# Performance work log

Measured on AMD Instinct MI355X. Metric: run time of the kernel, lower is better.

The kernel has to match this reference:

```python
import jax, jax.numpy as jnp
import numpy as np

WIDTH = [512, 512, 512, 512]
GRID_SIZE = 5
K = 3  # spline order
GRID_RANGE = (-1.0, 1.0)
BATCH = 1024


def extend_grid(grid, k):
    # grid: (I, G+1) -> (I, G+2k+1), extend k knots on each side with uniform step h
    h = (grid[:, -1:] - grid[:, :1]) / (grid.shape[1] - 1)
    for _ in range(k):
        grid = jnp.concatenate([grid[:, :1] - h, grid, grid[:, -1:] + h], axis=1)
    return grid


def b_spline_basis(x, grid, k):
    # Cox-de Boor recursion. x: (B, I), grid: (I, G+2k+1) -> (B, I, G+k)
    xe = x[:, :, None]
    g = grid[None, :, :]
    B = ((xe >= g[:, :, :-1]) & (xe < g[:, :, 1:])).astype(x.dtype)
    for p in range(1, k + 1):
        B = ((xe - g[:, :, :-(p + 1)]) / (g[:, :, p:-1] - g[:, :, :-(p + 1)]) * B[:, :, :-1]
             + (g[:, :, p + 1:] - xe) / (g[:, :, p + 1:] - g[:, :, 1:-p]) * B[:, :, 1:])
    return B


def kan_layer(x, grid, coef, sb, sp):
    # x: (B, I); coef: (I, O, G+k); sb, sp: (I, O)
    base = jax.nn.silu(x)                              # residual b(x), (B, I)
    Bmat = b_spline_basis(x, grid, K)                  # (B, I, G+k)
    y = jnp.einsum('bik,iok->bio', Bmat, coef)         # spline curves, (B, I, O)
    post = sb[None] * base[:, :, None] + sp[None] * y  # postacts (B, I, O)
    return post.sum(axis=1)                            # (B, O)


def setup_inputs() -> dict:
    key = jax.random.key(0)
    ks = jax.random.split(key, 1 + 2 * (len(WIDTH) - 1))
    inp = {"x": jax.random.normal(ks[0], (BATCH, WIDTH[0]), dtype=jnp.float32)}
    for l, (i, o) in enumerate(zip(WIDTH[:-1], WIDTH[1:])):
        base = jnp.linspace(GRID_RANGE[0], GRID_RANGE[1], GRID_SIZE + 1, dtype=jnp.float32)
        grid = extend_grid(jnp.broadcast_to(base[None], (i, GRID_SIZE + 1)), K)
        kc, kb = ks[1 + 2 * l], ks[2 + 2 * l]
        inp[f"grid{l}"] = grid
        inp[f"coef{l}"] = jax.random.normal(kc, (i, o, GRID_SIZE + K), dtype=jnp.float32) * (0.1 / GRID_SIZE)
        inp[f"sb{l}"] = (jax.random.uniform(kb, (i, o), dtype=jnp.float32) * 2.0 - 1.0) / np.sqrt(i).astype(np.float32)
        inp[f"sp{l}"] = jnp.ones((i, o), dtype=jnp.float32) / np.sqrt(i).astype(np.float32)
    return inp


def reference(x, grid0, coef0, sb0, sp0, grid1, coef1, sb1, sp1, grid2, coef2, sb2, sp2):
    x = kan_layer(x, grid0, coef0, sb0, sp0)
    x = kan_layer(x, grid1, coef1, sb1, sp1)
    x = kan_layer(x, grid2, coef2, sb2, sp2)
    return x
```

## Files before the change

kernel.cpp:

```cpp
#include <hip/hip_runtime.h>
#include <hip/hip_bf16.h>

#define I_DIM  512
#define O_DIM  512
#define NBATCH 1024
#define NSPL   8
#define KPI    12
#define KDIM   (I_DIM * KPI)
#define NGRID  12

typedef __attribute__((ext_vector_type(8))) short bf16x8;
typedef __attribute__((ext_vector_type(4))) float f32x4;

__device__ __forceinline__ void gload_lds16(const __hip_bfloat16* g, __hip_bfloat16* l) {
    __builtin_amdgcn_global_load_lds(
        (const __attribute__((address_space(1))) void*)g,
        (__attribute__((address_space(3))) void*)l, 16, 0, 0);
}

__global__ void build_wt_all(const float* __restrict__ c0, const float* __restrict__ b0, const float* __restrict__ p0,
                             const float* __restrict__ c1, const float* __restrict__ b1, const float* __restrict__ p1,
                             const float* __restrict__ c2, const float* __restrict__ b2, const float* __restrict__ p2,
                             __hip_bfloat16* __restrict__ Wt) {
    int l = blockIdx.y;
    const float* coef = l == 0 ? c0 : (l == 1 ? c1 : c2);
    const float* sb   = l == 0 ? b0 : (l == 1 ? b1 : b2);
    const float* sp   = l == 0 ? p0 : (l == 1 ? p1 : p2);
    __hip_bfloat16* W = Wt + (size_t)l * O_DIM * KDIM;

    int tid = blockIdx.x * blockDim.x + threadIdx.x;
    int i = tid & (I_DIM - 1);
    int o = tid >> 9;
    float sbv = sb[i * O_DIM + o];
    float spv = sp[i * O_DIM + o];
    const float* cf = coef + (size_t)(i * O_DIM + o) * NSPL;
    __align__(16) __hip_bfloat16 row[KPI];
#pragma unroll
    for (int k = 0; k < NSPL; ++k) row[k] = __float2bfloat16(spv * cf[k]);
    __hip_bfloat16 whi = __float2bfloat16(sbv);
    __hip_bfloat16 wlo = __float2bfloat16(sbv - __bfloat162float(whi));
    row[8]  = whi;
    row[9]  = wlo;
    row[10] = whi;
    row[11] = __float2bfloat16(0.0f);
    uint2* dst = (uint2*)(W + (size_t)o * KDIM + i * KPI);
    const uint2* src = (const uint2*)row;
    dst[0] = src[0]; dst[1] = src[1]; dst[2] = src[2];
}

#define SPLITK 8

__device__ __forceinline__ void features_core(float xv, const float* __restrict__ grid,
                                              int i, __hip_bfloat16* __restrict__ dst) {
    float g[NGRID];
#pragma unroll
    for (int j = 0; j < NGRID; ++j) g[j] = grid[i * NGRID + j];

    float B[NGRID - 1];
#pragma unroll
    for (int j = 0; j < NGRID - 1; ++j)
        B[j] = (xv >= g[j] && xv < g[j + 1]) ? 1.0f : 0.0f;
#pragma unroll
    for (int p = 1; p <= 3; ++p) {
#pragma unroll
        for (int j = 0; j < NGRID - 1 - p; ++j) {
            B[j] = (xv - g[j]) / (g[j + p] - g[j]) * B[j]
                 + (g[j + p + 1] - xv) / (g[j + p + 1] - g[j + 1]) * B[j + 1];
        }
    }
    float s = xv / (1.0f + __expf(-xv));
    __hip_bfloat16 shi = __float2bfloat16(s);
    __hip_bfloat16 slo = __float2bfloat16(s - __bfloat162float(shi));

    __align__(16) __hip_bfloat16 row[KPI];
#pragma unroll
    for (int k = 0; k < NSPL; ++k) row[k] = __float2bfloat16(B[k]);
    row[8]  = shi;
    row[9]  = shi;
    row[10] = slo;
    row[11] = __float2bfloat16(0.0f);

    uint2* d = (uint2*)dst;
    const uint2* srow = (const uint2*)row;
    d[0] = srow[0]; d[1] = srow[1]; d[2] = srow[2];
}

__global__ void build_features_x(const float* __restrict__ x,
                                 const float* __restrict__ grid,
                                 __hip_bfloat16* __restrict__ F) {
    int tid = blockIdx.x * blockDim.x + threadIdx.x;
    features_core(x[tid], grid, tid & (I_DIM - 1), F + (size_t)tid * KPI);
}

__global__ void build_features_sum(const float* __restrict__ P,
                                   const float* __restrict__ grid,
                                   __hip_bfloat16* __restrict__ F) {
    int tid = blockIdx.x * blockDim.x + threadIdx.x;
    float xv = 0.f;
#pragma unroll
    for (int s = 0; s < SPLITK; ++s) xv += P[(size_t)s * NBATCH * I_DIM + tid];
    features_core(xv, grid, tid & (I_DIM - 1), F + (size_t)tid * KPI);
}

__global__ void reduce_out(const float* __restrict__ P, float* __restrict__ out) {
    int tid = blockIdx.x * blockDim.x + threadIdx.x;
    float v = 0.f;
#pragma unroll
    for (int s = 0; s < SPLITK; ++s) v += P[(size_t)s * NBATCH * O_DIM + tid];
    out[tid] = v;
}

#define BM 64
#define BN 64
#define BK 64
#define KSEG (KDIM / SPLITK)

__global__ __launch_bounds__(256)
void gemm_kernel(const __hip_bfloat16* __restrict__ A,
                 const __hip_bfloat16* __restrict__ Wt,
                 float* __restrict__ P) {
    __shared__ __hip_bfloat16 lA[BM * BK];
    __shared__ __hip_bfloat16 lB[BN * BK];

    int bm = blockIdx.x;
    int bn = blockIdx.y;
    int ks = blockIdx.z;
    int tid = threadIdx.x;
    int lane = tid & 63;
    int wave = tid >> 6;
    int wr = (wave & 1) * 32;
    int wc = (wave >> 1) * 32;
    int q  = lane >> 4;
    int ln = lane & 15;

    f32x4 acc[2][2];
#pragma unroll
    for (int a = 0; a < 2; ++a)
#pragma unroll
        for (int b = 0; b < 2; ++b) acc[a][b] = (f32x4){0.f, 0.f, 0.f, 0.f};

    const __hip_bfloat16* Abase = A  + (size_t)(bm * BM) * KDIM + ks * KSEG;
    const __hip_bfloat16* Bbase = Wt + (size_t)(bn * BN) * KDIM + ks * KSEG;

    int cc0 = wave * 128 + lane;
    int cc1 = cc0 + 64;
    int r0 = cc0 >> 3, j0 = (cc0 & 7) ^ (r0 & 7);
    int r1 = cc1 >> 3, j1 = (cc1 & 7) ^ (r1 & 7);
    __hip_bfloat16* ldsA0 = lA + (size_t)(wave * 128) * 8;
    __hip_bfloat16* ldsA1 = lA + (size_t)(wave * 128 + 64) * 8;
    __hip_bfloat16* ldsB0 = lB + (size_t)(wave * 128) * 8;
    __hip_bfloat16* ldsB1 = lB + (size_t)(wave * 128 + 64) * 8;

    for (int kt = 0; kt < KSEG; kt += BK) {
        __syncthreads();
        gload_lds16(Abase + (size_t)r0 * KDIM + kt + j0 * 8, ldsA0);
        gload_lds16(Abase + (size_t)r1 * KDIM + kt + j1 * 8, ldsA1);
        gload_lds16(Bbase + (size_t)r0 * KDIM + kt + j0 * 8, ldsB0);
        gload_lds16(Bbase + (size_t)r1 * KDIM + kt + j1 * 8, ldsB1);
        __syncthreads();

#pragma unroll
        for (int kh = 0; kh < 2; ++kh) {
            bf16x8 af[2], bfr[2];
#pragma unroll
            for (int rt = 0; rt < 2; ++rt) {
                int row = wr + rt * 16 + ln;
                af[rt] = *(const bf16x8*)(lA + row * BK + (((kh * 4 + q) ^ (row & 7)) * 8));
            }
#pragma unroll
            for (int ct = 0; ct < 2; ++ct) {
                int row = wc + ct * 16 + ln;
                bfr[ct] = *(const bf16x8*)(lB + row * BK + (((kh * 4 + q) ^ (row & 7)) * 8));
            }
#pragma unroll
            for (int rt = 0; rt < 2; ++rt)
#pragma unroll
                for (int ct = 0; ct < 2; ++ct)
                    acc[rt][ct] = __builtin_amdgcn_mfma_f32_16x16x32_bf16(
                        af[rt], bfr[ct], acc[rt][ct], 0, 0, 0);
        }
    }

    float* Pp = P + (size_t)ks * NBATCH * O_DIM;
    int orow = bm * BM + wr;
    int ocol = bn * BN + wc + ln;
#pragma unroll
    for (int rt = 0; rt < 2; ++rt)
#pragma unroll
        for (int ct = 0; ct < 2; ++ct)
#pragma unroll
            for (int r = 0; r < 4; ++r)
                Pp[(size_t)(orow + rt * 16 + q * 4 + r) * O_DIM + ocol + ct * 16]
                    = acc[rt][ct][r];
}

extern "C" void kernel_launch(void* const* d_in, const int* in_sizes, int n_in,
                              void* d_out, int out_size, void* d_ws, size_t ws_size,
                              hipStream_t stream) {
    const float* x0      = (const float*)d_in[0];
    const float* grid[3] = {(const float*)d_in[1], (const float*)d_in[5], (const float*)d_in[9]};
    const float* coef[3] = {(const float*)d_in[2], (const float*)d_in[6], (const float*)d_in[10]};
    const float* sb[3]   = {(const float*)d_in[3], (const float*)d_in[7], (const float*)d_in[11]};
    const float* sp[3]   = {(const float*)d_in[4], (const float*)d_in[8], (const float*)d_in[12]};

    char* ws = (char*)d_ws;
    const size_t wt_bytes = (size_t)O_DIM * KDIM * sizeof(__hip_bfloat16);
    const size_t f_bytes  = (size_t)NBATCH * KDIM * sizeof(__hip_bfloat16);
    __hip_bfloat16* Wt = (__hip_bfloat16*)ws;
    __hip_bfloat16* F  = (__hip_bfloat16*)(ws + 3 * wt_bytes);
    float* P = (float*)(ws + 3 * wt_bytes + f_bytes);

    build_wt_all<<<dim3((I_DIM * O_DIM) / 256, 3), 256, 0, stream>>>(
        coef[0], sb[0], sp[0], coef[1], sb[1], sp[1], coef[2], sb[2], sp[2], Wt);

    build_features_x<<<(NBATCH * I_DIM) / 256, 256, 0, stream>>>(x0, grid[0], F);
    gemm_kernel<<<dim3(16, 8, SPLITK), 256, 0, stream>>>(F, Wt, P);

    for (int l = 1; l < 3; ++l) {
        build_features_sum<<<(NBATCH * I_DIM) / 256, 256, 0, stream>>>(P, grid[l], F);
        gemm_kernel<<<dim3(16, 8, SPLITK), 256, 0, stream>>>(F, Wt + (size_t)l * O_DIM * KDIM, P);
    }
    reduce_out<<<(NBATCH * O_DIM) / 256, 256, 0, stream>>>(P, (float*)d_out);
}
```

Before: 201.3 us.

## Enlarge GEMM tiles to 128x128, double split-K, fuse prep kernels

The GEMM block tile grows from 64x64 to 128x128, with each wave computing a 4x4 grid of MFMA tiles instead of 2x2, so each loaded fragment is reused more. Split-K is raised from 8 to 16 to keep enough blocks (8x4x16) in flight. The weight-build and first-layer feature kernels are merged into one launch. In exchange the partial-sum buffer P doubles, so the reduction passes read twice as much. The larger tile also raises register use and may lower occupancy.

```diff
diff --git a/kernel.cpp b/kernel.cpp
--- a/kernel.cpp
+++ b/kernel.cpp
@@ -8,6 +8,7 @@
 #define KPI    12
 #define KDIM   (I_DIM * KPI)
 #define NGRID  12
+#define SPLITK 16
 
 typedef __attribute__((ext_vector_type(8))) short bf16x8;
 typedef __attribute__((ext_vector_type(4))) float f32x4;
@@ -18,17 +19,10 @@
         (__attribute__((address_space(3))) void*)l, 16, 0, 0);
 }
 
-__global__ void build_wt_all(const float* __restrict__ c0, const float* __restrict__ b0, const float* __restrict__ p0,
-                             const float* __restrict__ c1, const float* __restrict__ b1, const float* __restrict__ p1,
-                             const float* __restrict__ c2, const float* __restrict__ b2, const float* __restrict__ p2,
-                             __hip_bfloat16* __restrict__ Wt) {
-    int l = blockIdx.y;
-    const float* coef = l == 0 ? c0 : (l == 1 ? c1 : c2);
-    const float* sb   = l == 0 ? b0 : (l == 1 ? b1 : b2);
-    const float* sp   = l == 0 ? p0 : (l == 1 ? p1 : p2);
-    __hip_bfloat16* W = Wt + (size_t)l * O_DIM * KDIM;
-
-    int tid = blockIdx.x * blockDim.x + threadIdx.x;
+__device__ __forceinline__ void wt_core(const float* __restrict__ coef,
+                                        const float* __restrict__ sb,
+                                        const float* __restrict__ sp,
+                                        __hip_bfloat16* __restrict__ W, int tid) {
     int i = tid & (I_DIM - 1);
     int o = tid >> 9;
     float sbv = sb[i * O_DIM + o];
@@ -48,8 +42,6 @@
     dst[0] = src[0]; dst[1] = src[1]; dst[2] = src[2];
 }
 
-#define SPLITK 8
-
 __device__ __forceinline__ void features_core(float xv, const float* __restrict__ grid,
                                               int i, __hip_bfloat16* __restrict__ dst) {
     float g[NGRID];
@@ -85,11 +77,23 @@
     d[0] = srow[0]; d[1] = srow[1]; d[2] = srow[2];
 }
 
-__global__ void build_features_x(const float* __restrict__ x,
-                                 const float* __restrict__ grid,
-                                 __hip_bfloat16* __restrict__ F) {
-    int tid = blockIdx.x * blockDim.x + threadIdx.x;
-    features_core(x[tid], grid, tid & (I_DIM - 1), F + (size_t)tid * KPI);
+__global__ void prep_kernel(const float* __restrict__ c0, const float* __restrict__ b0, const float* __restrict__ p0,
+                            const float* __restrict__ c1, const float* __restrict__ b1, const float* __restrict__ p1,
+                            const float* __restrict__ c2, const float* __restrict__ b2, const float* __restrict__ p2,
+                            __hip_bfloat16* __restrict__ Wt,
+                            const float* __restrict__ x, const float* __restrict__ grid0,
+                            __hip_bfloat16* __restrict__ F) {
+    if (blockIdx.x < 3072) {
+        int l = blockIdx.x / 1024;
+        const float* coef = l == 0 ? c0 : (l == 1 ? c1 : c2);
+        const float* sb   = l == 0 ? b0 : (l == 1 ? b1 : b2);
+        const float* sp   = l == 0 ? p0 : (l == 1 ? p1 : p2);
+        int tid = (blockIdx.x - l * 1024) * 256 + threadIdx.x;
+        wt_core(coef, sb, sp, Wt + (size_t)l * O_DIM * KDIM, tid);
+    } else {
+        int tid = (blockIdx.x - 3072) * 256 + threadIdx.x;
+        features_core(x[tid], grid0, tid & (I_DIM - 1), F + (size_t)tid * KPI);
+    }
 }
 
 __global__ void build_features_sum(const float* __restrict__ P,
@@ -110,8 +114,8 @@
     out[tid] = v;
 }
 
-#define BM 64
-#define BN 64
+#define BM 128
+#define BN 128
 #define BK 64
 #define KSEG (KDIM / SPLITK)
 
@@ -128,56 +132,58 @@
     int tid = threadIdx.x;
     int lane = tid & 63;
     int wave = tid >> 6;
-    int wr = (wave & 1) * 32;
-    int wc = (wave >> 1) * 32;
+    int wr = (wave & 1) * 64;
+    int wc = (wave >> 1) * 64;
     int q  = lane >> 4;
     int ln = lane & 15;
 
-    f32x4 acc[2][2];
-#pragma unroll
-    for (int a = 0; a < 2; ++a)
-#pragma unroll
-        for (int b = 0; b < 2; ++b) acc[a][b] = (f32x4){0.f, 0.f, 0.f, 0.f};
+    f32x4 acc[4][4];
+#pragma unroll
+    for (int a = 0; a < 4; ++a)
+#pragma unroll
+        for (int b = 0; b < 4; ++b) acc[a][b] = (f32x4){0.f, 0.f, 0.f, 0.f};
 
     const __hip_bfloat16* Abase = A  + (size_t)(bm * BM) * KDIM + ks * KSEG;
     const __hip_bfloat16* Bbase = Wt + (size_t)(bn * BN) * KDIM + ks * KSEG;
 
-    int cc0 = wave * 128 + lane;
-    int cc1 = cc0 + 64;
-    int r0 = cc0 >> 3, j0 = (cc0 & 7) ^ (r0 & 7);
-    int r1 = cc1 >> 3, j1 = (cc1 & 7) ^ (r1 & 7);
-    __hip_bfloat16* ldsA0 = lA + (size_t)(wave * 128) * 8;
-    __hip_bfloat16* ldsA1 = lA + (size_t)(wave * 128 + 64) * 8;
-    __hip_bfloat16* ldsB0 = lB + (size_t)(wave * 128) * 8;
-    __hip_bfloat16* ldsB1 = lB + (size_t)(wave * 128 + 64) * 8;
+    int ccw[4], rr[4], jj[4];
+#pragma unroll
+    for (int c = 0; c < 4; ++c) {
+        int cc = c * 256 + tid;
+        ccw[c] = c * 256 + wave * 64;
+        rr[c] = cc >> 3;
+        jj[c] = (cc & 7) ^ (rr[c] & 7);
+    }
 
     for (int kt = 0; kt < KSEG; kt += BK) {
         __syncthreads();
-        gload_lds16(Abase + (size_t)r0 * KDIM + kt + j0 * 8, ldsA0);
-        gload_lds16(Abase + (size_t)r1 * KDIM + kt + j1 * 8, ldsA1);
-        gload_lds16(Bbase + (size_t)r0 * KDIM + kt + j0 * 8, ldsB0);
-        gload_lds16(Bbase + (size_t)r1 * KDIM + kt + j1 * 8, ldsB1);
+#pragma unroll
+        for (int c = 0; c < 4; ++c)
+            gload_lds16(Abase + (size_t)rr[c] * KDIM + kt + jj[c] * 8, lA + ccw[c] * 8);
+#pragma unroll
+        for (int c = 0; c < 4; ++c)
+            gload_lds16(Bbase + (size_t)rr[c] * KDIM + kt + jj[c] * 8, lB + ccw[c] * 8);
         __syncthreads();
 
 #pragma unroll
         for (int kh = 0; kh < 2; ++kh) {
-            bf16x8 af[2], bfr[2];
-#pragma unroll
-            for (int rt = 0; rt < 2; ++rt) {
+            bf16x8 af[4], bf[4];
+#pragma unroll
+            for (int rt = 0; rt < 4; ++rt) {
                 int row = wr + rt * 16 + ln;
                 af[rt] = *(const bf16x8*)(lA + row * BK + (((kh * 4 + q) ^ (row & 7)) * 8));
             }
 #pragma unroll
-            for (int ct = 0; ct < 2; ++ct) {
+            for (int ct = 0; ct < 4; ++ct) {
                 int row = wc + ct * 16 + ln;
-                bfr[ct] = *(const bf16x8*)(lB + row * BK + (((kh * 4 + q) ^ (row & 7)) * 8));
+                bf[ct] = *(const bf16x8*)(lB + row * BK + (((kh * 4 + q) ^ (row & 7)) * 8));
             }
 #pragma unroll
-            for (int rt = 0; rt < 2; ++rt)
-#pragma unroll
-                for (int ct = 0; ct < 2; ++ct)
+            for (int rt = 0; rt < 4; ++rt)
+#pragma unroll
+                for (int ct = 0; ct < 4; ++ct)
                     acc[rt][ct] = __builtin_amdgcn_mfma_f32_16x16x32_bf16(
-                        af[rt], bfr[ct], acc[rt][ct], 0, 0, 0);
+                        af[rt], bf[ct], acc[rt][ct], 0, 0, 0);
         }
     }
 
@@ -185,9 +191,9 @@
     int orow = bm * BM + wr;
     int ocol = bn * BN + wc + ln;
 #pragma unroll
-    for (int rt = 0; rt < 2; ++rt)
-#pragma unroll
-        for (int ct = 0; ct < 2; ++ct)
+    for (int rt = 0; rt < 4; ++rt)
+#pragma unroll
+        for (int ct = 0; ct < 4; ++ct)
 #pragma unroll
             for (int r = 0; r < 4; ++r)
                 Pp[(size_t)(orow + rt * 16 + q * 4 + r) * O_DIM + ocol + ct * 16]
@@ -210,15 +216,14 @@
     __hip_bfloat16* F  = (__hip_bfloat16*)(ws + 3 * wt_bytes);
     float* P = (float*)(ws + 3 * wt_bytes + f_bytes);
 
-    build_wt_all<<<dim3((I_DIM * O_DIM) / 256, 3), 256, 0, stream>>>(
-        coef[0], sb[0], sp[0], coef[1], sb[1], sp[1], coef[2], sb[2], sp[2], Wt);
-
-    build_features_x<<<(NBATCH * I_DIM) / 256, 256, 0, stream>>>(x0, grid[0], F);
-    gemm_kernel<<<dim3(16, 8, SPLITK), 256, 0, stream>>>(F, Wt, P);
+    prep_kernel<<<5120, 256, 0, stream>>>(
+        coef[0], sb[0], sp[0], coef[1], sb[1], sp[1], coef[2], sb[2], sp[2],
+        Wt, x0, grid[0], F);
+    gemm_kernel<<<dim3(8, 4, SPLITK), 256, 0, stream>>>(F, Wt, P);
 
     for (int l = 1; l < 3; ++l) {
         build_features_sum<<<(NBATCH * I_DIM) / 256, 256, 0, stream>>>(P, grid[l], F);
-        gemm_kernel<<<dim3(16, 8, SPLITK), 256, 0, stream>>>(F, Wt + (size_t)l * O_DIM * KDIM, P);
+        gemm_kernel<<<dim3(8, 4, SPLITK), 256, 0, stream>>>(F, Wt + (size_t)l * O_DIM * KDIM, P);
     }
     reduce_out<<<(NBATCH * O_DIM) / 256, 256, 0, stream>>>(P, (float*)d_out);
 }
```

Result: slower. 215.1 us (+6.9%).
